# Kernel optimization log

Hardware: AMD Instinct MI355X
Metric: run time of the kernel (lower is better)

The kernel has to match this reference:

```python
import jax, jax.numpy as jnp
import numpy as np

WIDTH = 2048
NUM_HEADS = 16
HEAD_DIM = WIDTH // NUM_HEADS  # 128
ROPE_DIMS = HEAD_DIM // 2      # 64, partial rotary
WINDOW = 512
ROPE_BASE = 10000.0
NEG_INF = -1e9


def apply_rope(x, dims, offset=0, base=ROPE_BASE):
    # x: [B, H, L, hd]; non-traditional (half-split) rotary on first `dims` dims.
    L = x.shape[2]
    half = dims // 2
    pos = (offset + jnp.arange(L)).astype(x.dtype)                     # [L]
    inv_freq = jnp.exp(-jnp.log(jnp.asarray(base, x.dtype)) * (jnp.arange(0, dims, 2).astype(x.dtype) / dims))  # [half]
    theta = pos[:, None] * inv_freq[None, :]                           # [L, half]
    cos = jnp.cos(theta)[None, None]                                   # [1,1,L,half]
    sin = jnp.sin(theta)[None, None]
    x1 = x[..., :half]
    x2 = x[..., half:dims]
    rest = x[..., dims:]
    rx1 = x1 * cos - x2 * sin
    rx2 = x1 * sin + x2 * cos
    return jnp.concatenate([rx1, rx2, rest], axis=-1)


def setup_inputs() -> dict:
    key = jax.random.key(0)
    ks = jax.random.split(key, 6)
    B, L, D, hd = 2, 2048, WIDTH, HEAD_DIM
    x = jax.random.normal(ks[0], (B, L, D), dtype=jnp.float32)
    Wq = jax.random.normal(ks[1], (D, D), dtype=jnp.float32) * 0.02
    Wk = jax.random.normal(ks[2], (D, hd), dtype=jnp.float32) * 0.02
    Wv = jax.random.normal(ks[3], (D, hd), dtype=jnp.float32) * 0.02
    Wo = jax.random.normal(ks[4], (D, D), dtype=jnp.float32) * 0.02
    bo = jax.random.normal(ks[5], (D,), dtype=jnp.float32) * 0.02
    return {"x": x, "Wq": Wq, "Wk": Wk, "Wv": Wv, "Wo": Wo, "bo": bo}


def reference(x, Wq, Wk, Wv, Wo, bo):
    B, L, D = x.shape
    H, hd = NUM_HEADS, HEAD_DIM
    scale = hd ** (-0.5)

    q = (x @ Wq).reshape(B, L, H, hd).transpose(0, 2, 1, 3)   # [B,H,L,hd]
    k = (x @ Wk).reshape(B, L, 1, hd).transpose(0, 2, 1, 3)   # [B,1,L,hd] (MQA)
    v = (x @ Wv).reshape(B, L, 1, hd).transpose(0, 2, 1, 3)

    q = apply_rope(q, ROPE_DIMS)
    k = apply_rope(k, ROPE_DIMS)

    # sliding-window causal mask: attend iff 0 <= i - j < WINDOW
    i = jnp.arange(L)[:, None]
    j = jnp.arange(L)[None, :]
    allowed = (i - j >= 0) & (i - j < WINDOW)                  # [L,L]
    mask = jnp.where(allowed, 0.0, NEG_INF).astype(x.dtype)

    scores = jnp.einsum("bhqd,bkd->bhqk", q, k[:, 0]) * scale  # [B,H,L,L]
    scores = scores + mask[None, None]
    attn = jax.nn.softmax(scores, axis=-1)
    out = jnp.einsum("bhqk,bkd->bhqd", attn, v[:, 0])          # [B,H,L,hd]
    out = out.transpose(0, 2, 1, 3).reshape(B, L, D)
    return out @ Wo + bo
```

## Files before the change

kernel.cpp:

```cpp
#include <hip/hip_runtime.h>
#include <hip/hip_bf16.h>
#include <stdint.h>


typedef float  f32x4  __attribute__((ext_vector_type(4)));
typedef __bf16 bf16x8 __attribute__((ext_vector_type(8)));

#define ASYNC_LD16(gp, lp)                                                     \
  __builtin_amdgcn_global_load_lds(                                            \
      (__attribute__((address_space(1))) void*)(gp),                           \
      (__attribute__((address_space(3))) void*)(lp), 16, 0, 0)

__global__ __launch_bounds__(256) void prep_all(
    const float* __restrict__ x, __hip_bfloat16* __restrict__ xb,
    const float* __restrict__ Wq, const float* __restrict__ Wk,
    const float* __restrict__ Wv, const float* __restrict__ Wo,
    __hip_bfloat16* __restrict__ wqkvT, __hip_bfloat16* __restrict__ woT) {
  __shared__ float t[32][33];
  int bid = blockIdx.x;
  if (bid < 8192) {
    const int i = bid * 256 + threadIdx.x;
    const float4 v = ((const float4*)x)[i];
    __align__(8) __hip_bfloat16 o[4] = {
        __float2bfloat16(v.x), __float2bfloat16(v.y),
        __float2bfloat16(v.z), __float2bfloat16(v.w)};
    *(uint2*)(xb + (size_t)i * 4) = *(uint2*)o;
    return;
  }
  bid -= 8192;
  const float* src;
  __hip_bfloat16* dst;
  int C, cb, rb;
  if (bid < 4096) {
    src = Wq; dst = wqkvT; C = 2048; cb = bid & 63; rb = bid >> 6;
  } else if (bid < 4352) {
    const int l = bid - 4096;
    src = Wk; dst = wqkvT + 2048ull * 2048; C = 128; cb = l & 3; rb = l >> 2;
  } else if (bid < 4608) {
    const int l = bid - 4352;
    src = Wv; dst = wqkvT + 2176ull * 2048; C = 128; cb = l & 3; rb = l >> 2;
  } else {
    const int l = bid - 4608;
    src = Wo; dst = woT; C = 2048; cb = l & 63; rb = l >> 6;
  }
  const int c0 = cb * 32, r0 = rb * 32;
  const int r8 = threadIdx.x >> 3;
  const int c4 = (threadIdx.x & 7) << 2;
  const float4 v4 = *(const float4*)&src[(size_t)(r0 + r8) * C + c0 + c4];
  t[r8][c4 + 0] = v4.x;
  t[r8][c4 + 1] = v4.y;
  t[r8][c4 + 2] = v4.z;
  t[r8][c4 + 3] = v4.w;
  __syncthreads();
  __align__(8) __hip_bfloat16 o4[4];
  o4[0] = __float2bfloat16(t[c4 + 0][r8]);
  o4[1] = __float2bfloat16(t[c4 + 1][r8]);
  o4[2] = __float2bfloat16(t[c4 + 2][r8]);
  o4[3] = __float2bfloat16(t[c4 + 3][r8]);
  *(uint2*)&dst[(size_t)(c0 + r8) * 2048 + r0 + c4] = *(uint2*)o4;
}

__device__ __forceinline__ void xcd_remap(int& bx, int& by) {
  const int nwg = gridDim.x * gridDim.y;
  const int flat = blockIdx.y * gridDim.x + blockIdx.x;
  const int cpx = nwg >> 3;
  const int nid = (flat & 7) * cpx + (flat >> 3);
  bx = nid % gridDim.x;
  by = nid / gridDim.x;
}

__device__ __forceinline__ void gemm_core64(const __bf16* __restrict__ A,
                                            const __bf16* __restrict__ BT,
                                            int K, int m0, int n0, __bf16* As,
                                            __bf16* Bs, f32x4 (&acc)[2][4]) {
  const int tid = threadIdx.x;
  const int wave = tid >> 6;
  const int lane = tid & 63;
  const int wm = (wave & 1) * 32;
  const int wn = (wave >> 1) * 64;
  const int ln = lane & 15;
  const int quad = lane >> 4;
  const int rdoff = (quad ^ ((ln >> 1) & 3)) * 8;

  size_t goffA[2];
  int ldsoffA[2];
#pragma unroll
  for (int i = 0; i < 2; i++) {
    const int cidx = (wave * 2 + i) * 64 + lane;
    const int p = cidx >> 8;
    const int pidx = cidx & 255;
    const int row = pidx >> 2;
    const int cc = pidx & 3;
    const int cg = cc ^ ((row >> 1) & 3);
    goffA[i] = (size_t)row * K + p * 32 + cg * 8;
    ldsoffA[i] = (wave * 2 + i) * 512;
  }
  size_t goffB[4];
  int ldsoffB[4];
#pragma unroll
  for (int i = 0; i < 4; i++) {
    const int cidx = (wave * 4 + i) * 64 + lane;
    const int p = cidx >> 9;
    const int pidx = cidx & 511;
    const int row = pidx >> 2;
    const int cc = pidx & 3;
    const int cg = cc ^ ((row >> 1) & 3);
    goffB[i] = (size_t)row * K + p * 32 + cg * 8;
    ldsoffB[i] = (wave * 4 + i) * 512;
  }
  const __bf16* Abase = A + (size_t)m0 * K;
  const __bf16* Bbase = BT + (size_t)n0 * K;

  for (int k0 = 0; k0 < K; k0 += 64) {
#pragma unroll
    for (int i = 0; i < 2; i++)
      ASYNC_LD16(Abase + k0 + goffA[i], As + ldsoffA[i]);
#pragma unroll
    for (int i = 0; i < 4; i++)
      ASYNC_LD16(Bbase + k0 + goffB[i], Bs + ldsoffB[i]);
    __syncthreads();
    bf16x8 af[2][2], bf[4][2];
#pragma unroll
    for (int i = 0; i < 2; i++)
#pragma unroll
      for (int p = 0; p < 2; p++)
        af[i][p] = *(const bf16x8*)&As[p * 2048 + (wm + i * 16 + ln) * 32 + rdoff];
#pragma unroll
    for (int j = 0; j < 4; j++)
#pragma unroll
      for (int p = 0; p < 2; p++)
        bf[j][p] = *(const bf16x8*)&Bs[p * 4096 + (wn + j * 16 + ln) * 32 + rdoff];
#pragma unroll
    for (int p = 0; p < 2; p++)
#pragma unroll
      for (int i = 0; i < 2; i++)
#pragma unroll
        for (int j = 0; j < 4; j++)
          acc[i][j] = __builtin_amdgcn_mfma_f32_16x16x32_bf16(af[i][p], bf[j][p],
                                                              acc[i][j], 0, 0, 0);
    __syncthreads();
  }
}

__global__ __launch_bounds__(256) void gemm_qkv(
    const __bf16* __restrict__ A, const __bf16* __restrict__ BT,
    __hip_bfloat16* __restrict__ qd, __hip_bfloat16* __restrict__ kd,
    __hip_bfloat16* __restrict__ vtd, int K) {
  __shared__ __align__(16) __bf16 As[2 * 2048];
  __shared__ __align__(16) __bf16 Bs[2 * 4096];
  int bx, by;
  xcd_remap(bx, by);
  const int m0 = by * 64;
  const int n0 = bx * 128;
  f32x4 acc[2][4];
  const f32x4 zero = {0.f, 0.f, 0.f, 0.f};
#pragma unroll
  for (int i = 0; i < 2; i++)
#pragma unroll
    for (int j = 0; j < 4; j++) acc[i][j] = zero;
  gemm_core64(A, BT, K, m0, n0, As, Bs, acc);

  const int tid = threadIdx.x;
  const int wave = tid >> 6;
  const int lane = tid & 63;
  const int quad = lane >> 4;
  const int ln = lane & 15;
  const int wm = (wave & 1) * 32;
  const int wn = (wave >> 1) * 64;

  if (n0 == 2176) {
    const int bb = m0 >> 11;
    const int mloc = m0 & 2047;
#pragma unroll
    for (int i = 0; i < 2; i++) {
      const int rb = mloc + wm + i * 16 + quad * 4;
#pragma unroll
      for (int j = 0; j < 4; j++) {
        const int col = wn + j * 16 + ln;
        __align__(8) __hip_bfloat16 t4[4];
#pragma unroll
        for (int r = 0; r < 4; r++) t4[r] = __float2bfloat16(acc[i][j][r]);
        *(uint2*)(vtd + ((size_t)(bb * 128 + col)) * 2048 + rb) = *(uint2*)t4;
      }
    }
    return;
  }

  __hip_bfloat16* dst;
  int dstride, dcol;
  if (n0 < 2048) {
    dst = qd; dstride = 2048; dcol = n0;
  } else {
    dst = kd; dstride = 128; dcol = 0;
  }
  const bool dorope = (wn == 0);
  float invf0 = 0.f, invf1 = 0.f;
  if (dorope) {
    invf0 = expf(-0.28782313662425574f * (float)ln);
    invf1 = expf(-0.28782313662425574f * (float)(16 + ln));
  }

#pragma unroll
  for (int i = 0; i < 2; i++) {
#pragma unroll
    for (int r = 0; r < 4; r++) {
      const int row = m0 + wm + i * 16 + quad * 4 + r;
      float o0 = acc[i][0][r], o1 = acc[i][1][r];
      float o2 = acc[i][2][r], o3 = acc[i][3][r];
      if (dorope) {
        const float pos = (float)(row & 2047);
        float s0, c0, s1, c1;
        __sincosf(pos * invf0, &s0, &c0);
        __sincosf(pos * invf1, &s1, &c1);
        const float a0 = o0, b0 = o2, a1 = o1, b1 = o3;
        o0 = a0 * c0 - b0 * s0;
        o2 = a0 * s0 + b0 * c0;
        o1 = a1 * c1 - b1 * s1;
        o3 = a1 * s1 + b1 * c1;
      }
      __hip_bfloat16* rp = dst + (size_t)row * dstride + dcol + wn + ln;
      rp[0]  = __float2bfloat16(o0);
      rp[16] = __float2bfloat16(o1);
      rp[32] = __float2bfloat16(o2);
      rp[48] = __float2bfloat16(o3);
    }
  }
}

__global__ __launch_bounds__(256) void gemm_out(
    const __bf16* __restrict__ A, const __bf16* __restrict__ BT,
    float* __restrict__ C, const float* __restrict__ bias, int N, int K) {
  __shared__ __align__(16) __bf16 As[2 * 2048];
  __shared__ __align__(16) __bf16 Bs[2 * 4096];
  int bx, by;
  xcd_remap(bx, by);
  const int m0 = by * 64;
  const int n0 = bx * 128;
  f32x4 acc[2][4];
  const f32x4 zero = {0.f, 0.f, 0.f, 0.f};
#pragma unroll
  for (int i = 0; i < 2; i++)
#pragma unroll
    for (int j = 0; j < 4; j++) acc[i][j] = zero;
  gemm_core64(A, BT, K, m0, n0, As, Bs, acc);

  const int tid = threadIdx.x;
  const int wave = tid >> 6;
  const int lane = tid & 63;
  const int wm = (wave & 1) * 32;
  const int wn = (wave >> 1) * 64;
  const int lrow = lane & 15;
#pragma unroll
  for (int j = 0; j < 4; j++) {
    const int col = n0 + wn + j * 16 + lrow;
    const float bv = bias[col];
#pragma unroll
    for (int i = 0; i < 2; i++) {
#pragma unroll
      for (int r = 0; r < 4; r++) {
        const int row = m0 + wm + i * 16 + (lane >> 4) * 4 + r;
        C[(size_t)row * N + col] = acc[i][j][r] + bv;
      }
    }
  }
}

__global__ __launch_bounds__(512) void attn_mfma(
    const __bf16* __restrict__ qb,
    const __bf16* __restrict__ kb,
    const __bf16* __restrict__ vtb,
    __hip_bfloat16* __restrict__ o)
{
  __shared__ __align__(16) __bf16 Ks[2][4][64 * 32];
  __shared__ __align__(16) __bf16 Vs[2][2][128 * 32];
  __shared__ __align__(16) __bf16 Ps[8][2][512];
  const int tid = threadIdx.x;
  const int w = tid >> 6;
  const int lane = tid & 63;
  const int quad = lane >> 4;
  const int ln = lane & 15;
  const int bid = blockIdx.x;
  const int q0 = (bid & 15) * 128;
  const int h = (bid >> 4) & 15;
  const int b = bid >> 8;
  const int swr = (ln >> 1) & 3;
  const int rdoff = (quad ^ swr) * 8;

  bf16x8 qf[4];
  {
    const __bf16* qrow =
        qb + ((size_t)(b * 2048 + q0 + w * 16 + ln)) * 2048 + h * 128;
#pragma unroll
    for (int ks = 0; ks < 4; ks++)
      qf[ks] = *(const bf16x8*)(qrow + ks * 32 + quad * 8);
  }

  f32x4 oacc[8];
  const f32x4 zero = {0.f, 0.f, 0.f, 0.f};
#pragma unroll
  for (int nb = 0; nb < 8; nb++) oacc[nb] = zero;
  float li[4] = {0.f, 0.f, 0.f, 0.f};
  const float scale = 0.08838834764831845f;

  const __bf16* kbase = kb + (size_t)b * 2048 * 128;
  const __bf16* vbase = vtb + (size_t)b * 128 * 2048;

  const int key4 = lane >> 2, uu = lane & 3;
  const int sw = (key4 >> 1) & 3;

  auto stage_kv = [&](int t, int bufi) {
    const int jt = q0 - 512 + 64 * t;
#pragma unroll
    for (int i = 0; i < 4; ++i) {
      const int g = w * 4 + i;
      if (g < 16) {
        const int ks = g & 3, keybase = (g >> 2) * 16;
        ASYNC_LD16(kbase + (size_t)(jt + keybase + key4) * 128 + ks * 32 +
                       (uu ^ sw) * 8,
                   &Ks[bufi][ks][keybase * 32]);
      } else {
        const int c = g - 16;
        const int p = c & 1, dbase = (c >> 1) * 16;
        ASYNC_LD16(vbase + (size_t)(dbase + key4) * 2048 + jt + p * 32 +
                       (uu ^ sw) * 8,
                   &Vs[bufi][p][dbase * 32]);
      }
    }
  };

#define SOFTMAX_BODY(MASKED)                                                   \
  _Pragma("unroll") for (int j = 0; j < 4; j++)                                \
  _Pragma("unroll") for (int r = 0; r < 4; r++) {                              \
    float v = sacc[j][r] * scale;                                              \
    if (MASKED) {                                                              \
      const int d0 = (w * 16 + quad * 4 + r) - (j * 16 + ln);                  \
      if (t <= 1 && d0 >= (t << 6)) v = -1e30f;                                \
      if (t >= 8 && d0 < ((t - 8) << 6)) v = -1e30f;                           \
    }                                                                          \
    v = fminf(v, 60.f);                                                        \
    const float p = __expf(v);                                                 \
    li[r] += p;                                                                \
    const int ch = (j & 1) * 2 + (ln >> 3);                                    \
    const int swp = (quad * 2 + (r >> 1)) & 3;                                 \
    Ps[w][j >> 1][(quad * 4 + r) * 32 + (ch ^ swp) * 8 + (ln & 7)] =           \
        (__bf16)p;                                                             \
  }

  const int tstart = (q0 >= 512) ? 0 : (512 - q0) / 64;
  int cur = 0;
  stage_kv(tstart, 0);
  for (int t = tstart; t < 10; ++t) {
    __syncthreads();
    if (t + 1 < 10) stage_kv(t + 1, cur ^ 1);

    f32x4 sacc[4];
#pragma unroll
    for (int j = 0; j < 4; j++) sacc[j] = zero;
    __builtin_amdgcn_s_setprio(1);
#pragma unroll
    for (int j = 0; j < 4; j++)
#pragma unroll
      for (int ks = 0; ks < 4; ks++) {
        const bf16x8 kf =
            *(const bf16x8*)&Ks[cur][ks][(j * 16 + ln) * 32 + rdoff];
        sacc[j] = __builtin_amdgcn_mfma_f32_16x16x32_bf16(qf[ks], kf, sacc[j],
                                                          0, 0, 0);
      }
    __builtin_amdgcn_s_setprio(0);

    if (t <= 1 || t >= 8) {
      SOFTMAX_BODY(1)
    } else {
      SOFTMAX_BODY(0)
    }

    const bf16x8 pf0 = *(const bf16x8*)&Ps[w][0][ln * 32 + rdoff];
    const bf16x8 pf1 = *(const bf16x8*)&Ps[w][1][ln * 32 + rdoff];
    __builtin_amdgcn_s_setprio(1);
#pragma unroll
    for (int nb = 0; nb < 8; nb++) {
      const bf16x8 vf0 =
          *(const bf16x8*)&Vs[cur][0][(nb * 16 + ln) * 32 + rdoff];
      const bf16x8 vf1 =
          *(const bf16x8*)&Vs[cur][1][(nb * 16 + ln) * 32 + rdoff];
      oacc[nb] = __builtin_amdgcn_mfma_f32_16x16x32_bf16(pf0, vf0, oacc[nb],
                                                         0, 0, 0);
      oacc[nb] = __builtin_amdgcn_mfma_f32_16x16x32_bf16(pf1, vf1, oacc[nb],
                                                         0, 0, 0);
    }
    __builtin_amdgcn_s_setprio(0);
    cur ^= 1;
  }
#undef SOFTMAX_BODY

#pragma unroll
  for (int off = 1; off < 16; off <<= 1)
#pragma unroll
    for (int r = 0; r < 4; r++) li[r] += __shfl_xor(li[r], off);

  __hip_bfloat16* obase =
      o + ((size_t)(b * 2048 + q0 + w * 16 + quad * 4)) * 2048 + h * 128 + ln;
#pragma unroll
  for (int r = 0; r < 4; r++) {
    const float inv = 1.0f / li[r];
#pragma unroll
    for (int nb = 0; nb < 8; nb++)
      obase[(size_t)r * 2048 + nb * 16] = __float2bfloat16(oacc[nb][r] * inv);
  }
}

extern "C" void kernel_launch(void* const* d_in, const int* in_sizes, int n_in,
                              void* d_out, int out_size, void* d_ws,
                              size_t ws_size, hipStream_t stream) {
  const float* x = (const float*)d_in[0];
  const float* Wq = (const float*)d_in[1];
  const float* Wk = (const float*)d_in[2];
  const float* Wv = (const float*)d_in[3];
  const float* Wo = (const float*)d_in[4];
  const float* bo = (const float*)d_in[5];
  float* out = (float*)d_out;

  char* w = (char*)d_ws;
  auto alloc = [&](size_t bytes) {
    void* p = (void*)w;
    w += (bytes + 255) & ~(size_t)255;
    return p;
  };
  __bf16* xb = (__bf16*)alloc(4096ull * 2048 * 2);
  __hip_bfloat16* wqkvT = (__hip_bfloat16*)alloc(2304ull * 2048 * 2);
  __hip_bfloat16* woT = (__hip_bfloat16*)alloc(2048ull * 2048 * 2);
  __hip_bfloat16* qbuf = (__hip_bfloat16*)alloc(4096ull * 2048 * 2);
  __hip_bfloat16* kbuf = (__hip_bfloat16*)alloc(4096ull * 128 * 2);
  __hip_bfloat16* vtb = (__hip_bfloat16*)alloc(4096ull * 128 * 2);
  __hip_bfloat16* attnb = (__hip_bfloat16*)xb;

  prep_all<<<16896, 256, 0, stream>>>(x, (__hip_bfloat16*)xb, Wq, Wk, Wv, Wo,
                                      wqkvT, woT);

  gemm_qkv<<<dim3(18, 64), 256, 0, stream>>>(xb, (const __bf16*)wqkvT, qbuf,
                                             kbuf, vtb, 2048);

  attn_mfma<<<512, 512, 0, stream>>>((const __bf16*)qbuf, (const __bf16*)kbuf,
                                     (const __bf16*)vtb, attnb);

  gemm_out<<<dim3(16, 64), 256, 0, stream>>>((const __bf16*)attnb,
                                             (const __bf16*)woT, out, bo, 2048,
                                             2048);
}
```

Before: 245.1 us.

## Double-buffer LDS tiles in GEMM core to overlap loads with MFMA

Replaces the single-buffered K loop in the shared GEMM core with a ping-pong LDS scheme. The next K tile's async global-to-LDS loads are issued before the current tile's MFMAs, and there is one barrier per iteration instead of two. The goal is to hide global load latency behind compute in both the QKV and output projections. In exchange, each block's LDS allocation doubles (to 48KB as declared), which may reduce how many blocks fit per CU.

```diff
diff --git a/kernel.cpp b/kernel.cpp
--- a/kernel.cpp
+++ b/kernel.cpp
@@ -69,10 +69,11 @@
   by = nid / gridDim.x;
 }
 
-__device__ __forceinline__ void gemm_core64(const __bf16* __restrict__ A,
-                                            const __bf16* __restrict__ BT,
-                                            int K, int m0, int n0, __bf16* As,
-                                            __bf16* Bs, f32x4 (&acc)[2][4]) {
+__device__ __forceinline__ void gemm_core64_db(const __bf16* __restrict__ A,
+                                               const __bf16* __restrict__ BT,
+                                               int K, int m0, int n0,
+                                               __bf16* As, __bf16* Bs,
+                                               f32x4 (&acc)[2][4]) {
   const int tid = threadIdx.x;
   const int wave = tid >> 6;
   const int lane = tid & 63;
@@ -110,35 +111,51 @@
   }
   const __bf16* Abase = A + (size_t)m0 * K;
   const __bf16* Bbase = BT + (size_t)n0 * K;
-
-  for (int k0 = 0; k0 < K; k0 += 64) {
+  const int NT = K >> 6;
+
+#pragma unroll
+  for (int i = 0; i < 2; i++) ASYNC_LD16(Abase + goffA[i], As + ldsoffA[i]);
+#pragma unroll
+  for (int i = 0; i < 4; i++) ASYNC_LD16(Bbase + goffB[i], Bs + ldsoffB[i]);
+
+  int cur = 0;
+  for (int t = 0; t < NT; ++t) {
+    __syncthreads();
+    if (t + 1 < NT) {
+      const int k0 = (t + 1) << 6;
+      __bf16* an = As + ((cur ^ 1) << 12);
+      __bf16* bn = Bs + ((cur ^ 1) << 13);
+#pragma unroll
+      for (int i = 0; i < 2; i++)
+        ASYNC_LD16(Abase + k0 + goffA[i], an + ldsoffA[i]);
+#pragma unroll
+      for (int i = 0; i < 4; i++)
+        ASYNC_LD16(Bbase + k0 + goffB[i], bn + ldsoffB[i]);
+    }
+    const __bf16* as_ = As + (cur << 12);
+    const __bf16* bs_ = Bs + (cur << 13);
+    bf16x8 af[2][2], bf[4][2];
 #pragma unroll
     for (int i = 0; i < 2; i++)
-      ASYNC_LD16(Abase + k0 + goffA[i], As + ldsoffA[i]);
-#pragma unroll
-    for (int i = 0; i < 4; i++)
-      ASYNC_LD16(Bbase + k0 + goffB[i], Bs + ldsoffB[i]);
-    __syncthreads();
-    bf16x8 af[2][2], bf[4][2];
-#pragma unroll
-    for (int i = 0; i < 2; i++)
 #pragma unroll
       for (int p = 0; p < 2; p++)
-        af[i][p] = *(const bf16x8*)&As[p * 2048 + (wm + i * 16 + ln) * 32 + rdoff];
+        af[i][p] =
+            *(const bf16x8*)&as_[p * 2048 + (wm + i * 16 + ln) * 32 + rdoff];
 #pragma unroll
     for (int j = 0; j < 4; j++)
 #pragma unroll
       for (int p = 0; p < 2; p++)
-        bf[j][p] = *(const bf16x8*)&Bs[p * 4096 + (wn + j * 16 + ln) * 32 + rdoff];
+        bf[j][p] =
+            *(const bf16x8*)&bs_[p * 4096 + (wn + j * 16 + ln) * 32 + rdoff];
 #pragma unroll
     for (int p = 0; p < 2; p++)
 #pragma unroll
       for (int i = 0; i < 2; i++)
 #pragma unroll
         for (int j = 0; j < 4; j++)
-          acc[i][j] = __builtin_amdgcn_mfma_f32_16x16x32_bf16(af[i][p], bf[j][p],
-                                                              acc[i][j], 0, 0, 0);
-    __syncthreads();
+          acc[i][j] = __builtin_amdgcn_mfma_f32_16x16x32_bf16(
+              af[i][p], bf[j][p], acc[i][j], 0, 0, 0);
+    cur ^= 1;
   }
 }
 
@@ -146,8 +163,8 @@
     const __bf16* __restrict__ A, const __bf16* __restrict__ BT,
     __hip_bfloat16* __restrict__ qd, __hip_bfloat16* __restrict__ kd,
     __hip_bfloat16* __restrict__ vtd, int K) {
-  __shared__ __align__(16) __bf16 As[2 * 2048];
-  __shared__ __align__(16) __bf16 Bs[2 * 4096];
+  __shared__ __align__(16) __bf16 As[2 * 4096];
+  __shared__ __align__(16) __bf16 Bs[2 * 8192];
   int bx, by;
   xcd_remap(bx, by);
   const int m0 = by * 64;
@@ -158,7 +175,7 @@
   for (int i = 0; i < 2; i++)
 #pragma unroll
     for (int j = 0; j < 4; j++) acc[i][j] = zero;
-  gemm_core64(A, BT, K, m0, n0, As, Bs, acc);
+  gemm_core64_db(A, BT, K, m0, n0, As, Bs, acc);
 
   const int tid = threadIdx.x;
   const int wave = tid >> 6;
@@ -230,8 +247,8 @@
 __global__ __launch_bounds__(256) void gemm_out(
     const __bf16* __restrict__ A, const __bf16* __restrict__ BT,
     float* __restrict__ C, const float* __restrict__ bias, int N, int K) {
-  __shared__ __align__(16) __bf16 As[2 * 2048];
-  __shared__ __align__(16) __bf16 Bs[2 * 4096];
+  __shared__ __align__(16) __bf16 As[2 * 4096];
+  __shared__ __align__(16) __bf16 Bs[2 * 8192];
   int bx, by;
   xcd_remap(bx, by);
   const int m0 = by * 64;
@@ -242,7 +259,7 @@
   for (int i = 0; i < 2; i++)
 #pragma unroll
     for (int j = 0; j < 4; j++) acc[i][j] = zero;
-  gemm_core64(A, BT, K, m0, n0, As, Bs, acc);
+  gemm_core64_db(A, BT, K, m0, n0, As, Bs, acc);
 
   const int tid = threadIdx.x;
   const int wave = tid >> 6;
```

Result: slower. 260.9 us (+6.4%).
